# Optimization experiments

Measured on AMD Instinct MI355X. Metric: run time of the kernel, lower is better.

## Reference

```python
import jax, jax.numpy as jnp
import numpy as np

N_NODES = 100000
N_EDGES = 1600000
F_IN = 128
HID = 128


def setup_inputs() -> dict:
    key = jax.random.key(0)
    ks = jax.random.split(key, 10)
    x = jax.random.normal(ks[0], (N_NODES, F_IN), dtype=jnp.float32)
    edge_index = jax.random.randint(ks[1], (2, N_EDGES), 0, N_NODES, dtype=jnp.int64)
    edge_weight = jax.random.uniform(ks[2], (N_EDGES,), dtype=jnp.float32)
    # Glorot-style params for the three GCNConv layers (conv_mid reused twice)
    W_in = jax.random.normal(ks[3], (F_IN, HID), dtype=jnp.float32) / np.sqrt(F_IN)
    b_in = jnp.zeros((HID,), dtype=jnp.float32)
    W_mid = jax.random.normal(ks[4], (HID, HID), dtype=jnp.float32) / np.sqrt(HID)
    b_mid = jnp.zeros((HID,), dtype=jnp.float32)
    W_fin = jax.random.normal(ks[5], (HID, 1), dtype=jnp.float32) / np.sqrt(HID)
    b_fin = jnp.zeros((1,), dtype=jnp.float32)
    return {"x": x, "edge_index": edge_index, "edge_weight": edge_weight,
            "W_in": W_in, "b_in": b_in, "W_mid": W_mid, "b_mid": b_mid,
            "W_fin": W_fin, "b_fin": b_fin}


def _gcn_norm(edge_index, edge_weight, n_nodes):
    """PyG GCNConv normalization with implicit self-loops (weight 1).
    Returns (edge_norm [E], self_norm [N]) where self_norm = 1/deg."""
    dst = edge_index[1]
    deg = jax.ops.segment_sum(edge_weight, dst, num_segments=n_nodes) + 1.0
    dinv = jnp.where(deg > 0, jax.lax.rsqrt(deg), 0.0)  # deg^-1/2
    edge_norm = dinv[edge_index[0]] * edge_weight * dinv[dst]
    self_norm = dinv * dinv  # self-loop: dinv[i] * 1 * dinv[i]
    return edge_norm, self_norm


def _gcn_conv(x, edge_index, edge_norm, self_norm, W, b, n_nodes):
    h = x @ W  # [N, out]
    msgs = edge_norm[:, None] * h[edge_index[0]]  # [E, out]
    agg = jax.ops.segment_sum(msgs, edge_index[1], num_segments=n_nodes)
    return agg + self_norm[:, None] * h + b


def reference(x, edge_index, edge_weight, W_in, b_in, W_mid, b_mid, W_fin, b_fin):
    n = x.shape[0]
    edge_norm, self_norm = _gcn_norm(edge_index, edge_weight, n)
    h = jax.nn.relu(_gcn_conv(x, edge_index, edge_norm, self_norm, W_in, b_in, n))
    h = jax.nn.relu(_gcn_conv(h, edge_index, edge_norm, self_norm, W_mid, b_mid, n))
    h = jax.nn.relu(_gcn_conv(h, edge_index, edge_norm, self_norm, W_mid, b_mid, n))
    out = _gcn_conv(h, edge_index, edge_norm, self_norm, W_fin, b_fin, n)
    return out  # [N, 1]
```

## Files before the change

### kernel.cpp

```cpp
#include <hip/hip_runtime.h>
#include <stdint.h>

#define N_NODES 100000
#define N_EDGES 1600000
#define F 128
#define CBN 512
#define NCBK 196
#define CHUNK 4096
#define BUFCAP 10240

typedef _Float16 f16;
typedef _Float16 f16x4 __attribute__((ext_vector_type(4)));
typedef _Float16 f16x8 __attribute__((ext_vector_type(8)));
typedef float f32x4 __attribute__((ext_vector_type(4)));

__device__ inline float unpackw(unsigned int p) {
    unsigned short b = (unsigned short)(p & 0x7FFF);
    return (float)__builtin_bit_cast(f16, b);
}


__global__ void k_zero0(int* bktcnt, unsigned int* edges) {
    int i = threadIdx.x;
    if (i < NCBK) bktcnt[i] = 0;
    if (i >= 248) edges[N_EDGES + (i - 248)] = 0u;
}

__launch_bounds__(256)
__global__ void k_bhist(const int* __restrict__ ei, int* __restrict__ bktcnt, int e) {
    __shared__ int h[NCBK];
    int tid = threadIdx.x;
    if (tid < NCBK) h[tid] = 0;
    __syncthreads();
    int base = blockIdx.x * CHUNK;
    int cnt = min(CHUNK, e - base);
    const int* dst = ei + N_EDGES + base;
    if (cnt == CHUNK) {
        const int4* d4 = (const int4*)dst;
#pragma unroll
        for (int k = 0; k < 4; k++) {
            int4 v = d4[tid + k * 256];
            atomicAdd(&h[v.x >> 9], 1);
            atomicAdd(&h[v.y >> 9], 1);
            atomicAdd(&h[v.z >> 9], 1);
            atomicAdd(&h[v.w >> 9], 1);
        }
    } else {
        for (int i = tid; i < cnt; i += 256)
            atomicAdd(&h[dst[i] >> 9], 1);
    }
    __syncthreads();
    if (tid < NCBK && h[tid]) atomicAdd(&bktcnt[tid], h[tid]);
}

__launch_bounds__(256)
__global__ void k_bktscan(const int* __restrict__ bktcnt, int* __restrict__ gbase,
                          int* __restrict__ gcur, int* __restrict__ row) {
    __shared__ int ls[256];
    int tid = threadIdx.x;
    int v = (tid < NCBK) ? bktcnt[tid] : 0;
    ls[tid] = v;
    __syncthreads();
    for (int off = 1; off < 256; off <<= 1) {
        int t = (tid >= off) ? ls[tid - off] : 0;
        __syncthreads();
        ls[tid] += t;
        __syncthreads();
    }
    int ex = ls[tid] - v;
    if (tid < NCBK) { gbase[tid] = ex; gcur[tid] = ex; }
    if (tid == NCBK) gbase[NCBK] = N_EDGES;
    if (tid == 0) row[N_NODES] = N_EDGES;
}


__launch_bounds__(256)
__global__ void k_binA(const int* __restrict__ ei, const float* __restrict__ w,
                       int* __restrict__ gcur, int2* __restrict__ stage, int e) {
    __shared__ int hist[256];
    __shared__ int bst[257];
    __shared__ int gb[256];
    __shared__ int ls[256];
    __shared__ int rec[CHUNK];
    __shared__ int meta[CHUNK];
    int tid = threadIdx.x;
    int base = blockIdx.x * CHUNK;
    int cnt = min(CHUNK, e - base);
    hist[tid] = 0;
    __syncthreads();

    int ew_[16], mr_[16];
    int nloc = 0;
    if (cnt == CHUNK) {
#pragma unroll
        for (int k = 0; k < 16; k++) {
            int i = base + tid + k * 256;
            int s = ei[i];
            int d = ei[N_EDGES + i];
            f16 hw = (f16)w[i];
            unsigned short wb = __builtin_bit_cast(unsigned short, hw);
            ew_[k] = (int)(((unsigned int)s << 15) | (wb & 0x7FFF));
            int cb = d >> 9;
            int local = d & (CBN - 1);
            int r = atomicAdd(&hist[cb], 1);
            mr_[k] = (cb << 22) | (local << 13) | r;
        }
        nloc = 16;
    } else {
        for (int i = tid; i < cnt; i += 256) {
            int s = ei[base + i];
            int d = ei[N_EDGES + base + i];
            f16 hw = (f16)w[base + i];
            unsigned short wb = __builtin_bit_cast(unsigned short, hw);
            ew_[nloc] = (int)(((unsigned int)s << 15) | (wb & 0x7FFF));
            int cb = d >> 9;
            int local = d & (CBN - 1);
            int r = atomicAdd(&hist[cb], 1);
            mr_[nloc] = (cb << 22) | (local << 13) | r;
            nloc++;
        }
    }
    __syncthreads();
    int v = hist[tid];
    ls[tid] = v;
    __syncthreads();
    for (int off = 1; off < 256; off <<= 1) {
        int t = (tid >= off) ? ls[tid - off] : 0;
        __syncthreads();
        ls[tid] += t;
        __syncthreads();
    }
    bst[tid] = ls[tid] - v;
    if (tid == 255) bst[256] = ls[255];
    __syncthreads();
    for (int k = 0; k < nloc; k++) {
        int m = mr_[k];
        int cb = m >> 22;
        int pos = bst[cb] + (m & 0x1FFF);
        rec[pos] = ew_[k];
        meta[pos] = (cb << 9) | ((m >> 13) & 0x1FF);
    }
    __syncthreads();
    if (tid < NCBK) {
        int c = bst[tid + 1] - bst[tid];
        gb[tid] = c ? atomicAdd(&gcur[tid], c) : 0;
    }
    __syncthreads();
    for (int j = tid; j < cnt; j += 256) {
        int m = meta[j];
        int cb = m >> 9;
        stage[gb[cb] + (j - bst[cb])] = make_int2(m & 511, rec[j]);
    }
}

__launch_bounds__(256)
__global__ void k_binB(const int2* __restrict__ stage, const int* __restrict__ gbase,
                       unsigned int* __restrict__ edges, int* __restrict__ row,
                       float* __restrict__ dinv) {
    __shared__ int cnt[CBN];
    __shared__ int ex[CBN + 1];
    __shared__ int cur[CBN];
    __shared__ int ls[256];
    __shared__ unsigned int buf[BUFCAP];
    int tid = threadIdx.x;
    int cb = blockIdx.x;
    int n0 = cb * CBN;
    int nn = min(CBN, N_NODES - n0);
    int base = gbase[cb];
    int hi = gbase[cb + 1];
    cnt[tid] = 0;
    cnt[tid + 256] = 0;
    __syncthreads();
    for (int j = base + tid; j < hi; j += 256)
        atomicAdd(&cnt[stage[j].x], 1);
    __syncthreads();
    int a = cnt[2 * tid], b = cnt[2 * tid + 1];
    int s = a + b;
    ls[tid] = s;
    __syncthreads();
    for (int off = 1; off < 256; off <<= 1) {
        int t = (tid >= off) ? ls[tid - off] : 0;
        __syncthreads();
        ls[tid] += t;
        __syncthreads();
    }
    int bx = ls[tid] - s;
    ex[2 * tid] = bx;
    ex[2 * tid + 1] = bx + a;
    cur[2 * tid] = bx;
    cur[2 * tid + 1] = bx + a;
    if (tid == 255) ex[512] = ls[255];
    __syncthreads();
    for (int l = tid; l < nn; l += 256) row[n0 + l] = base + ex[l];
    for (int j = base + tid; j < hi; j += 256) {
        int2 r = stage[j];
        int p = atomicAdd(&cur[r.x], 1);
        buf[p] = (unsigned int)r.y;
    }
    __syncthreads();
    int range = hi - base;
    for (int j = tid; j < range; j += 256)
        edges[base + j] = buf[j];
    for (int l = tid; l < nn; l += 256) {
        int lo = ex[l];
        int h2 = ex[l + 1];
        float sm = 1.0f;
        for (int j = lo; j < h2; j++) sm += unpackw(buf[j]);
        dinv[n0 + l] = rsqrtf(sm);
    }
}


__global__ void k_cvt(const float* __restrict__ X, f16* __restrict__ Y, int n8) {
    int i = blockIdx.x * blockDim.x + threadIdx.x;
    if (i < n8) {
        float4 a = ((const float4*)X)[i * 2];
        float4 b = ((const float4*)X)[i * 2 + 1];
        f16x8 o;
        o[0] = (f16)a.x; o[1] = (f16)a.y; o[2] = (f16)a.z; o[3] = (f16)a.w;
        o[4] = (f16)b.x; o[5] = (f16)b.y; o[6] = (f16)b.z; o[7] = (f16)b.w;
        ((f16x8*)Y)[i] = o;
    }
}

__global__ void k_wt2(const float* __restrict__ Wa, const float* __restrict__ Wb,
                      f16* __restrict__ Wta, f16* __restrict__ Wtb) {
    const float* W = blockIdx.x ? Wb : Wa;
    f16* Wt = blockIdx.x ? Wtb : Wta;
    int t = threadIdx.x;
#pragma unroll
    for (int it = 0; it < 64; it++) {
        int idx = t + it * 256;
        int k = idx >> 7, n = idx & 127;
        Wt[n * 128 + k] = (f16)W[idx];
    }
}


#define LDK 136

__launch_bounds__(256, 2)
__global__ void k_gemm16(const f16* __restrict__ A, const f16* __restrict__ Wt,
                         const float* __restrict__ dinv, f16* __restrict__ H, int nrows) {
    __shared__ f16 Ws[128 * LDK];
    int tid = threadIdx.x;
    int r0 = blockIdx.x * 128;
    int wave = tid >> 6;
    int lane = tid & 63;
    int lrow = lane & 15;
    int quad = lane >> 4;

    f16x8 a[2][4];
#pragma unroll
    for (int mt = 0; mt < 2; mt++) {
        int row = r0 + wave * 32 + mt * 16 + lrow;
#pragma unroll
        for (int kc = 0; kc < 4; kc++) {
            if (row < nrows)
                a[mt][kc] = *(const f16x8*)&A[(size_t)row * F + kc * 32 + quad * 8];
            else
                a[mt][kc] = (f16x8){};
        }
    }
#pragma unroll
    for (int it = 0; it < 8; it++) {
        int c = tid + it * 256;
        int rw = c >> 4;
        int off = (c & 15) * 8;
        *(f16x8*)&Ws[rw * LDK + off] = *(const f16x8*)&Wt[rw * 128 + off];
    }
    __syncthreads();

    f32x4 acc[2][8] = {};
#pragma unroll
    for (int kc = 0; kc < 4; kc++) {
        f16x8 b[8];
#pragma unroll
        for (int nt = 0; nt < 8; nt++)
            b[nt] = *(const f16x8*)&Ws[(nt * 16 + lrow) * LDK + kc * 32 + quad * 8];
#pragma unroll
        for (int nt = 0; nt < 8; nt++) {
            acc[0][nt] = __builtin_amdgcn_mfma_f32_16x16x32_f16(a[0][kc], b[nt], acc[0][nt], 0, 0, 0);
            acc[1][nt] = __builtin_amdgcn_mfma_f32_16x16x32_f16(a[1][kc], b[nt], acc[1][nt], 0, 0, 0);
        }
    }
    __syncthreads();
#pragma unroll
    for (int mt = 0; mt < 2; mt++) {
#pragma unroll
        for (int r = 0; r < 4; r++) {
            int lr = wave * 32 + mt * 16 + quad * 4 + r;
            int grow = r0 + lr;
            float dv = (grow < nrows) ? dinv[grow] : 0.f;
#pragma unroll
            for (int nt = 0; nt < 8; nt++)
                Ws[lr * 132 + nt * 16 + lrow] = (f16)(acc[mt][nt][r] * dv);
        }
    }
    __syncthreads();
#pragma unroll
    for (int it = 0; it < 8; it++) {
        int c = it * 256 + tid;
        int rw = c >> 4;
        int col = (c & 15) * 8;
        int grow = r0 + rw;
        if (grow < nrows)
            *(f16x8*)&H[(size_t)grow * F + col] = *(const f16x8*)&Ws[rw * 132 + col];
    }
}


__launch_bounds__(256)
__global__ void k_agg(const f16* __restrict__ H16, const int* __restrict__ row,
                      const unsigned int* __restrict__ edges,
                      const float* __restrict__ dinv, const float* __restrict__ bias,
                      f16* __restrict__ out, int n) {
    int node = blockIdx.x * 16 + (threadIdx.x >> 4);
    if (node >= n) return;
    int sub = threadIdx.x & 15;
    int beg = row[node], end = row[node + 1];
    float acc0[8] = {}, acc1[8] = {}, acc2[8] = {}, acc3[8] = {};
    for (int t = (beg & ~3); t < end; t += 8) {
        uint4 ea = *(const uint4*)&edges[t];
        uint4 eb = *(const uint4*)&edges[t + 4];
        unsigned int e[8] = {ea.x, ea.y, ea.z, ea.w, eb.x, eb.y, eb.z, eb.w};
        float w[8];
        unsigned int srcw[8];
#pragma unroll
        for (int k = 0; k < 8; k++) {
            bool live = (t + k >= beg) && (t + k < end);
            w[k] = live ? unpackw(e[k]) : 0.f;
            srcw[k] = (t + k < end) ? e[k] : ea.x;
        }
        f16x8 v[8];
#pragma unroll
        for (int k = 0; k < 8; k++)
            v[k] = *(const f16x8*)&H16[(size_t)(srcw[k] >> 15) * F + sub * 8];
#pragma unroll
        for (int j = 0; j < 8; j++) {
            acc0[j] = fmaf(w[0], (float)v[0][j], acc0[j]);
            acc1[j] = fmaf(w[1], (float)v[1][j], acc1[j]);
            acc2[j] = fmaf(w[2], (float)v[2][j], acc2[j]);
            acc3[j] = fmaf(w[3], (float)v[3][j], acc3[j]);
            acc0[j] = fmaf(w[4], (float)v[4][j], acc0[j]);
            acc1[j] = fmaf(w[5], (float)v[5][j], acc1[j]);
            acc2[j] = fmaf(w[6], (float)v[6][j], acc2[j]);
            acc3[j] = fmaf(w[7], (float)v[7][j], acc3[j]);
        }
    }
    float dd = dinv[node];
    f16x8 h = *(const f16x8*)&H16[(size_t)node * F + sub * 8];
    float4 b0 = *(const float4*)&bias[sub * 8];
    float4 b1 = *(const float4*)&bias[sub * 8 + 4];
    float bb[8] = {b0.x, b0.y, b0.z, b0.w, b1.x, b1.y, b1.z, b1.w};
    f16x8 o;
#pragma unroll
    for (int j = 0; j < 8; j++) {
        float a = acc0[j] + acc1[j] + acc2[j] + acc3[j] + (float)h[j];
        o[j] = (f16)fmaxf(fmaf(dd, a, bb[j]), 0.f);
    }
    *(f16x8*)&out[(size_t)node * F + sub * 8] = o;
}

__launch_bounds__(256)
__global__ void k_agg_dot(const f16* __restrict__ H16, const int* __restrict__ row,
                          const unsigned int* __restrict__ edges,
                          const float* __restrict__ dinv, const float* __restrict__ bias,
                          const float* __restrict__ Wf, float* __restrict__ sout, int n) {
    int node = blockIdx.x * 16 + (threadIdx.x >> 4);
    if (node >= n) return;
    int sub = threadIdx.x & 15;
    int beg = row[node], end = row[node + 1];
    float acc0[8] = {}, acc1[8] = {}, acc2[8] = {}, acc3[8] = {};
    for (int t = (beg & ~3); t < end; t += 8) {
        uint4 ea = *(const uint4*)&edges[t];
        uint4 eb = *(const uint4*)&edges[t + 4];
        unsigned int e[8] = {ea.x, ea.y, ea.z, ea.w, eb.x, eb.y, eb.z, eb.w};
        float w[8];
        unsigned int srcw[8];
#pragma unroll
        for (int k = 0; k < 8; k++) {
            bool live = (t + k >= beg) && (t + k < end);
            w[k] = live ? unpackw(e[k]) : 0.f;
            srcw[k] = (t + k < end) ? e[k] : ea.x;
        }
        f16x8 v[8];
#pragma unroll
        for (int k = 0; k < 8; k++)
            v[k] = *(const f16x8*)&H16[(size_t)(srcw[k] >> 15) * F + sub * 8];
#pragma unroll
        for (int j = 0; j < 8; j++) {
            acc0[j] = fmaf(w[0], (float)v[0][j], acc0[j]);
            acc1[j] = fmaf(w[1], (float)v[1][j], acc1[j]);
            acc2[j] = fmaf(w[2], (float)v[2][j], acc2[j]);
            acc3[j] = fmaf(w[3], (float)v[3][j], acc3[j]);
            acc0[j] = fmaf(w[4], (float)v[4][j], acc0[j]);
            acc1[j] = fmaf(w[5], (float)v[5][j], acc1[j]);
            acc2[j] = fmaf(w[6], (float)v[6][j], acc2[j]);
            acc3[j] = fmaf(w[7], (float)v[7][j], acc3[j]);
        }
    }
    float dd = dinv[node];
    f16x8 h = *(const f16x8*)&H16[(size_t)node * F + sub * 8];
    float4 b0 = *(const float4*)&bias[sub * 8];
    float4 b1 = *(const float4*)&bias[sub * 8 + 4];
    float bb[8] = {b0.x, b0.y, b0.z, b0.w, b1.x, b1.y, b1.z, b1.w};
    float4 w0v = *(const float4*)&Wf[sub * 8];
    float4 w1v = *(const float4*)&Wf[sub * 8 + 4];
    float ww[8] = {w0v.x, w0v.y, w0v.z, w0v.w, w1v.x, w1v.y, w1v.z, w1v.w};
    float p = 0.f;
#pragma unroll
    for (int j = 0; j < 8; j++) {
        float a = acc0[j] + acc1[j] + acc2[j] + acc3[j] + (float)h[j];
        p += fmaxf(fmaf(dd, a, bb[j]), 0.f) * ww[j];
    }
    p += __shfl_xor(p, 8, 64);
    p += __shfl_xor(p, 4, 64);
    p += __shfl_xor(p, 2, 64);
    p += __shfl_xor(p, 1, 64);
    if (sub == 0) sout[node] = dd * p;
}

__global__ void k_aggs(const float* __restrict__ s, const int* __restrict__ row,
                       const unsigned int* __restrict__ edges,
                       const float* __restrict__ dinv, const float* __restrict__ bf,
                       float* __restrict__ out, int n) {
    int i = blockIdx.x * blockDim.x + threadIdx.x;
    if (i >= n) return;
    float dd = dinv[i];
    float ae = s[i];
    int beg = row[i], end = row[i + 1];
    for (int j = beg; j < end; j++) {
        unsigned int p = edges[j];
        ae = fmaf(unpackw(p), s[p >> 15], ae);
    }
    out[i] = fmaf(dd, ae, bf[0]);
}


extern "C" void kernel_launch(void* const* d_in, const int* in_sizes, int n_in,
                              void* d_out, int out_size, void* d_ws, size_t ws_size,
                              hipStream_t stream) {
    const float* x    = (const float*)d_in[0];
    const int*   ei   = (const int*)d_in[1];
    const float* ew   = (const float*)d_in[2];
    const float* Win  = (const float*)d_in[3];
    const float* bin  = (const float*)d_in[4];
    const float* Wmid = (const float*)d_in[5];
    const float* bmid = (const float*)d_in[6];
    const float* Wfin = (const float*)d_in[7];
    const float* bfin = (const float*)d_in[8];
    float* out = (float*)d_out;

    char* ws = (char*)d_ws;
    size_t off = 0;
    auto alloc = [&](size_t bytes) -> char* {
        char* p = ws + off;
        off = (off + bytes + 255) & ~(size_t)255;
        return p;
    };
    float* dinv  = (float*)alloc((size_t)N_NODES * 4);
    int*   row   = (int*)alloc((size_t)(N_NODES + 1) * 4);
    unsigned int* edges = (unsigned int*)alloc((size_t)(N_EDGES + 8) * 4);
    int*   bktcnt = (int*)alloc(256 * 4);
    int*   gbase  = (int*)alloc(256 * 4);
    int*   gcur   = (int*)alloc(256 * 4);
    f16*   wtin  = (f16*)alloc(128 * 128 * 2);
    f16*   wtmid = (f16*)alloc(128 * 128 * 2);
    f16*   H16   = (f16*)alloc((size_t)N_NODES * F * 2);
    f16*   AB16  = (f16*)alloc((size_t)N_NODES * F * 2);
    int2* stage = (int2*)H16;
    float* sbuf = (float*)AB16;

    dim3 b256(256);
    int gN = (N_NODES + 255) / 256;
    int gW = (N_NODES + 15) / 16;
    int gG = (N_NODES + 127) / 128;
    int n8 = N_NODES * F / 8;
    int gC = (n8 + 255) / 256;
    int gA = (N_EDGES + CHUNK - 1) / CHUNK;

    hipLaunchKernelGGL(k_zero0, dim3(1), b256, 0, stream, bktcnt, edges);
    hipLaunchKernelGGL(k_bhist, dim3(gA), b256, 0, stream, ei, bktcnt, N_EDGES);
    hipLaunchKernelGGL(k_bktscan, dim3(1), b256, 0, stream, bktcnt, gbase, gcur, row);
    hipLaunchKernelGGL(k_binA, dim3(gA), b256, 0, stream, ei, ew, gcur, stage, N_EDGES);
    hipLaunchKernelGGL(k_binB, dim3(NCBK), b256, 0, stream, stage, gbase, edges, row, dinv);
    hipLaunchKernelGGL(k_cvt, dim3(gC), b256, 0, stream, x, AB16, n8);
    hipLaunchKernelGGL(k_wt2, dim3(2), b256, 0, stream, Win, Wmid, wtin, wtmid);

    hipLaunchKernelGGL(k_gemm16, dim3(gG), b256, 0, stream, AB16, wtin, dinv, H16, N_NODES);
    hipLaunchKernelGGL(k_agg, dim3(gW), b256, 0, stream, H16, row, edges, dinv, bin, AB16, N_NODES);
    hipLaunchKernelGGL(k_gemm16, dim3(gG), b256, 0, stream, AB16, wtmid, dinv, H16, N_NODES);
    hipLaunchKernelGGL(k_agg, dim3(gW), b256, 0, stream, H16, row, edges, dinv, bmid, AB16, N_NODES);
    hipLaunchKernelGGL(k_gemm16, dim3(gG), b256, 0, stream, AB16, wtmid, dinv, H16, N_NODES);
    hipLaunchKernelGGL(k_agg_dot, dim3(gW), b256, 0, stream, H16, row, edges, dinv, bmid, Wfin, sbuf, N_NODES);
    hipLaunchKernelGGL(k_aggs, dim3(gN), b256, 0, stream, sbuf, row, edges, dinv, bfin, out, N_NODES);
}
```

Baseline: 409.6 us.

## Use fixed-capacity buckets to drop histogram/scan and fuse fp32 convert into GEMM

Edge binning now writes into fixed-capacity per-bucket slots counted via an atomic cursor, removing the histogram and scan kernels and storing per-node begin/end pairs. The first GEMM reads fp32 features directly and converts in registers, eliminating the separate conversion kernel and its intermediate buffer traffic. This relies on no bucket exceeding BUFCAP edges and enlarges the edge array with gaps.

Result: faster. 387.4 us (-5.4%).

```diff
diff --git a/kernel.cpp b/kernel.cpp
--- a/kernel.cpp
+++ b/kernel.cpp
@@ -20,57 +20,10 @@
 }
 
 
-__global__ void k_zero0(int* bktcnt, unsigned int* edges) {
+__global__ void k_zero0(int* gcur, unsigned int* edges) {
     int i = threadIdx.x;
-    if (i < NCBK) bktcnt[i] = 0;
-    if (i >= 248) edges[N_EDGES + (i - 248)] = 0u;
-}
-
-__launch_bounds__(256)
-__global__ void k_bhist(const int* __restrict__ ei, int* __restrict__ bktcnt, int e) {
-    __shared__ int h[NCBK];
-    int tid = threadIdx.x;
-    if (tid < NCBK) h[tid] = 0;
-    __syncthreads();
-    int base = blockIdx.x * CHUNK;
-    int cnt = min(CHUNK, e - base);
-    const int* dst = ei + N_EDGES + base;
-    if (cnt == CHUNK) {
-        const int4* d4 = (const int4*)dst;
-#pragma unroll
-        for (int k = 0; k < 4; k++) {
-            int4 v = d4[tid + k * 256];
-            atomicAdd(&h[v.x >> 9], 1);
-            atomicAdd(&h[v.y >> 9], 1);
-            atomicAdd(&h[v.z >> 9], 1);
-            atomicAdd(&h[v.w >> 9], 1);
-        }
-    } else {
-        for (int i = tid; i < cnt; i += 256)
-            atomicAdd(&h[dst[i] >> 9], 1);
-    }
-    __syncthreads();
-    if (tid < NCBK && h[tid]) atomicAdd(&bktcnt[tid], h[tid]);
-}
-
-__launch_bounds__(256)
-__global__ void k_bktscan(const int* __restrict__ bktcnt, int* __restrict__ gbase,
-                          int* __restrict__ gcur, int* __restrict__ row) {
-    __shared__ int ls[256];
-    int tid = threadIdx.x;
-    int v = (tid < NCBK) ? bktcnt[tid] : 0;
-    ls[tid] = v;
-    __syncthreads();
-    for (int off = 1; off < 256; off <<= 1) {
-        int t = (tid >= off) ? ls[tid - off] : 0;
-        __syncthreads();
-        ls[tid] += t;
-        __syncthreads();
-    }
-    int ex = ls[tid] - v;
-    if (tid < NCBK) { gbase[tid] = ex; gcur[tid] = ex; }
-    if (tid == NCBK) gbase[NCBK] = N_EDGES;
-    if (tid == 0) row[N_NODES] = N_EDGES;
+    if (i < NCBK) gcur[i] = 0;
+    if (i >= 248) edges[(size_t)NCBK * BUFCAP + (i - 248)] = 0u;
 }
 
 
@@ -149,13 +102,13 @@
     for (int j = tid; j < cnt; j += 256) {
         int m = meta[j];
         int cb = m >> 9;
-        stage[gb[cb] + (j - bst[cb])] = make_int2(m & 511, rec[j]);
+        stage[(size_t)cb * BUFCAP + gb[cb] + (j - bst[cb])] = make_int2(m & 511, rec[j]);
     }
 }
 
 __launch_bounds__(256)
-__global__ void k_binB(const int2* __restrict__ stage, const int* __restrict__ gbase,
-                       unsigned int* __restrict__ edges, int* __restrict__ row,
+__global__ void k_binB(const int2* __restrict__ stage, const int* __restrict__ gcur,
+                       unsigned int* __restrict__ edges, int2* __restrict__ row2,
                        float* __restrict__ dinv) {
     __shared__ int cnt[CBN];
     __shared__ int ex[CBN + 1];
@@ -166,13 +119,13 @@
     int cb = blockIdx.x;
     int n0 = cb * CBN;
     int nn = min(CBN, N_NODES - n0);
-    int base = gbase[cb];
-    int hi = gbase[cb + 1];
+    size_t sbase = (size_t)cb * BUFCAP;
+    int ecnt = gcur[cb];
     cnt[tid] = 0;
     cnt[tid + 256] = 0;
     __syncthreads();
-    for (int j = base + tid; j < hi; j += 256)
-        atomicAdd(&cnt[stage[j].x], 1);
+    for (int j = tid; j < ecnt; j += 256)
+        atomicAdd(&cnt[stage[sbase + j].x], 1);
     __syncthreads();
     int a = cnt[2 * tid], b = cnt[2 * tid + 1];
     int s = a + b;
@@ -191,16 +144,16 @@
     cur[2 * tid + 1] = bx + a;
     if (tid == 255) ex[512] = ls[255];
     __syncthreads();
-    for (int l = tid; l < nn; l += 256) row[n0 + l] = base + ex[l];
-    for (int j = base + tid; j < hi; j += 256) {
-        int2 r = stage[j];
+    for (int l = tid; l < nn; l += 256)
+        row2[n0 + l] = make_int2((int)sbase + ex[l], (int)sbase + ex[l + 1]);
+    for (int j = tid; j < ecnt; j += 256) {
+        int2 r = stage[sbase + j];
         int p = atomicAdd(&cur[r.x], 1);
         buf[p] = (unsigned int)r.y;
     }
     __syncthreads();
-    int range = hi - base;
-    for (int j = tid; j < range; j += 256)
-        edges[base + j] = buf[j];
+    for (int j = tid; j < ecnt; j += 256)
+        edges[sbase + j] = buf[j];
     for (int l = tid; l < nn; l += 256) {
         int lo = ex[l];
         int h2 = ex[l + 1];
@@ -210,18 +163,6 @@
     }
 }
 
-
-__global__ void k_cvt(const float* __restrict__ X, f16* __restrict__ Y, int n8) {
-    int i = blockIdx.x * blockDim.x + threadIdx.x;
-    if (i < n8) {
-        float4 a = ((const float4*)X)[i * 2];
-        float4 b = ((const float4*)X)[i * 2 + 1];
-        f16x8 o;
-        o[0] = (f16)a.x; o[1] = (f16)a.y; o[2] = (f16)a.z; o[3] = (f16)a.w;
-        o[4] = (f16)b.x; o[5] = (f16)b.y; o[6] = (f16)b.z; o[7] = (f16)b.w;
-        ((f16x8*)Y)[i] = o;
-    }
-}
 
 __global__ void k_wt2(const float* __restrict__ Wa, const float* __restrict__ Wb,
                       f16* __restrict__ Wta, f16* __restrict__ Wtb) {
@@ -309,16 +250,93 @@
     }
 }
 
+__launch_bounds__(256, 2)
+__global__ void k_gemmf(const float* __restrict__ A, const f16* __restrict__ Wt,
+                        const float* __restrict__ dinv, f16* __restrict__ H, int nrows) {
+    __shared__ f16 Ws[128 * LDK];
+    int tid = threadIdx.x;
+    int r0 = blockIdx.x * 128;
+    int wave = tid >> 6;
+    int lane = tid & 63;
+    int lrow = lane & 15;
+    int quad = lane >> 4;
+
+    f16x8 a[2][4];
+#pragma unroll
+    for (int mt = 0; mt < 2; mt++) {
+        int row = r0 + wave * 32 + mt * 16 + lrow;
+#pragma unroll
+        for (int kc = 0; kc < 4; kc++) {
+            if (row < nrows) {
+                float4 lo = *(const float4*)&A[(size_t)row * F + kc * 32 + quad * 8];
+                float4 hi = *(const float4*)&A[(size_t)row * F + kc * 32 + quad * 8 + 4];
+                f16x8 f;
+                f[0] = (f16)lo.x; f[1] = (f16)lo.y; f[2] = (f16)lo.z; f[3] = (f16)lo.w;
+                f[4] = (f16)hi.x; f[5] = (f16)hi.y; f[6] = (f16)hi.z; f[7] = (f16)hi.w;
+                a[mt][kc] = f;
+            } else {
+                a[mt][kc] = (f16x8){};
+            }
+        }
+    }
+#pragma unroll
+    for (int it = 0; it < 8; it++) {
+        int c = tid + it * 256;
+        int rw = c >> 4;
+        int off = (c & 15) * 8;
+        *(f16x8*)&Ws[rw * LDK + off] = *(const f16x8*)&Wt[rw * 128 + off];
+    }
+    __syncthreads();
+
+    f32x4 acc[2][8] = {};
+#pragma unroll
+    for (int kc = 0; kc < 4; kc++) {
+        f16x8 b[8];
+#pragma unroll
+        for (int nt = 0; nt < 8; nt++)
+            b[nt] = *(const f16x8*)&Ws[(nt * 16 + lrow) * LDK + kc * 32 + quad * 8];
+#pragma unroll
+        for (int nt = 0; nt < 8; nt++) {
+            acc[0][nt] = __builtin_amdgcn_mfma_f32_16x16x32_f16(a[0][kc], b[nt], acc[0][nt], 0, 0, 0);
+            acc[1][nt] = __builtin_amdgcn_mfma_f32_16x16x32_f16(a[1][kc], b[nt], acc[1][nt], 0, 0, 0);
+        }
+    }
+    __syncthreads();
+#pragma unroll
+    for (int mt = 0; mt < 2; mt++) {
+#pragma unroll
+        for (int r = 0; r < 4; r++) {
+            int lr = wave * 32 + mt * 16 + quad * 4 + r;
+            int grow = r0 + lr;
+            float dv = (grow < nrows) ? dinv[grow] : 0.f;
+#pragma unroll
+            for (int nt = 0; nt < 8; nt++)
+                Ws[lr * 132 + nt * 16 + lrow] = (f16)(acc[mt][nt][r] * dv);
+        }
+    }
+    __syncthreads();
+#pragma unroll
+    for (int it = 0; it < 8; it++) {
+        int c = it * 256 + tid;
+        int rw = c >> 4;
+        int col = (c & 15) * 8;
+        int grow = r0 + rw;
+        if (grow < nrows)
+            *(f16x8*)&H[(size_t)grow * F + col] = *(const f16x8*)&Ws[rw * 132 + col];
+    }
+}
+
 
 __launch_bounds__(256)
-__global__ void k_agg(const f16* __restrict__ H16, const int* __restrict__ row,
+__global__ void k_agg(const f16* __restrict__ H16, const int2* __restrict__ row2,
                       const unsigned int* __restrict__ edges,
                       const float* __restrict__ dinv, const float* __restrict__ bias,
                       f16* __restrict__ out, int n) {
     int node = blockIdx.x * 16 + (threadIdx.x >> 4);
     if (node >= n) return;
     int sub = threadIdx.x & 15;
-    int beg = row[node], end = row[node + 1];
+    int2 rr = row2[node];
+    int beg = rr.x, end = rr.y;
     float acc0[8] = {}, acc1[8] = {}, acc2[8] = {}, acc3[8] = {};
     for (int t = (beg & ~3); t < end; t += 8) {
         uint4 ea = *(const uint4*)&edges[t];
@@ -363,14 +381,15 @@
 }
 
 __launch_bounds__(256)
-__global__ void k_agg_dot(const f16* __restrict__ H16, const int* __restrict__ row,
+__global__ void k_agg_dot(const f16* __restrict__ H16, const int2* __restrict__ row2,
                           const unsigned int* __restrict__ edges,
                           const float* __restrict__ dinv, const float* __restrict__ bias,
                           const float* __restrict__ Wf, float* __restrict__ sout, int n) {
     int node = blockIdx.x * 16 + (threadIdx.x >> 4);
     if (node >= n) return;
     int sub = threadIdx.x & 15;
-    int beg = row[node], end = row[node + 1];
+    int2 rr = row2[node];
+    int beg = rr.x, end = rr.y;
     float acc0[8] = {}, acc1[8] = {}, acc2[8] = {}, acc3[8] = {};
     for (int t = (beg & ~3); t < end; t += 8) {
         uint4 ea = *(const uint4*)&edges[t];
@@ -421,7 +440,7 @@
     if (sub == 0) sout[node] = dd * p;
 }
 
-__global__ void k_aggs(const float* __restrict__ s, const int* __restrict__ row,
+__global__ void k_aggs(const float* __restrict__ s, const int2* __restrict__ row2,
                        const unsigned int* __restrict__ edges,
                        const float* __restrict__ dinv, const float* __restrict__ bf,
                        float* __restrict__ out, int n) {
@@ -429,8 +448,8 @@
     if (i >= n) return;
     float dd = dinv[i];
     float ae = s[i];
-    int beg = row[i], end = row[i + 1];
-    for (int j = beg; j < end; j++) {
+    int2 rr = row2[i];
+    for (int j = rr.x; j < rr.y; j++) {
         unsigned int p = edges[j];
         ae = fmaf(unpackw(p), s[p >> 15], ae);
     }
@@ -460,11 +479,9 @@
         return p;
     };
     float* dinv  = (float*)alloc((size_t)N_NODES * 4);
-    int*   row   = (int*)alloc((size_t)(N_NODES + 1) * 4);
-    unsigned int* edges = (unsigned int*)alloc((size_t)(N_EDGES + 8) * 4);
-    int*   bktcnt = (int*)alloc(256 * 4);
-    int*   gbase  = (int*)alloc(256 * 4);
-    int*   gcur   = (int*)alloc(256 * 4);
+    int2*  row2  = (int2*)alloc((size_t)N_NODES * 8);
+    unsigned int* edges = (unsigned int*)alloc(((size_t)NCBK * BUFCAP + 8) * 4);
+    int*   gcur  = (int*)alloc(256 * 4);
     f16*   wtin  = (f16*)alloc(128 * 128 * 2);
     f16*   wtmid = (f16*)alloc(128 * 128 * 2);
     f16*   H16   = (f16*)alloc((size_t)N_NODES * F * 2);
@@ -476,23 +493,18 @@
     int gN = (N_NODES + 255) / 256;
     int gW = (N_NODES + 15) / 16;
     int gG = (N_NODES + 127) / 128;
-    int n8 = N_NODES * F / 8;
-    int gC = (n8 + 255) / 256;
     int gA = (N_EDGES + CHUNK - 1) / CHUNK;
 
-    hipLaunchKernelGGL(k_zero0, dim3(1), b256, 0, stream, bktcnt, edges);
-    hipLaunchKernelGGL(k_bhist, dim3(gA), b256, 0, stream, ei, bktcnt, N_EDGES);
-    hipLaunchKernelGGL(k_bktscan, dim3(1), b256, 0, stream, bktcnt, gbase, gcur, row);
+    hipLaunchKernelGGL(k_zero0, dim3(1), b256, 0, stream, gcur, edges);
     hipLaunchKernelGGL(k_binA, dim3(gA), b256, 0, stream, ei, ew, gcur, stage, N_EDGES);
-    hipLaunchKernelGGL(k_binB, dim3(NCBK), b256, 0, stream, stage, gbase, edges, row, dinv);
-    hipLaunchKernelGGL(k_cvt, dim3(gC), b256, 0, stream, x, AB16, n8);
+    hipLaunchKernelGGL(k_binB, dim3(NCBK), b256, 0, stream, stage, gcur, edges, row2, dinv);
     hipLaunchKernelGGL(k_wt2, dim3(2), b256, 0, stream, Win, Wmid, wtin, wtmid);
 
-    hipLaunchKernelGGL(k_gemm16, dim3(gG), b256, 0, stream, AB16, wtin, dinv, H16, N_NODES);
-    hipLaunchKernelGGL(k_agg, dim3(gW), b256, 0, stream, H16, row, edges, dinv, bin, AB16, N_NODES);
+    hipLaunchKernelGGL(k_gemmf, dim3(gG), b256, 0, stream, x, wtin, dinv, H16, N_NODES);
+    hipLaunchKernelGGL(k_agg, dim3(gW), b256, 0, stream, H16, row2, edges, dinv, bin, AB16, N_NODES);
     hipLaunchKernelGGL(k_gemm16, dim3(gG), b256, 0, stream, AB16, wtmid, dinv, H16, N_NODES);
-    hipLaunchKernelGGL(k_agg, dim3(gW), b256, 0, stream, H16, row, edges, dinv, bmid, AB16, N_NODES);
+    hipLaunchKernelGGL(k_agg, dim3(gW), b256, 0, stream, H16, row2, edges, dinv, bmid, AB16, N_NODES);
     hipLaunchKernelGGL(k_gemm16, dim3(gG), b256, 0, stream, AB16, wtmid, dinv, H16, N_NODES);
-    hipLaunchKernelGGL(k_agg_dot, dim3(gW), b256, 0, stream, H16, row, edges, dinv, bmid, Wfin, sbuf, N_NODES);
-    hipLaunchKernelGGL(k_aggs, dim3(gN), b256, 0, stream, sbuf, row, edges, dinv, bfin, out, N_NODES);
-}
+    hipLaunchKernelGGL(k_agg_dot, dim3(gW), b256, 0, stream, H16, row2, edges, dinv, bmid, Wfin, sbuf, N_NODES);
+    hipLaunchKernelGGL(k_aggs, dim3(gN), b256, 0, stream, sbuf, row2, edges, dinv, bfin, out, N_NODES);
+}
```
